# Kernel optimization log

Hardware: AMD Instinct MI355X
Metric: run time of the kernel (lower is better)

Reference implementation:

```python
import jax, jax.numpy as jnp
import numpy as np

K = 16          # knn neighbors (init kwarg k)
GROUPS = 4      # GroupNorm groups
EPS = 1e-5
SLOPE = 0.2     # LeakyReLU negative slope


def fps(xyz, n):
    """Farthest point sampling. xyz: (B,N,3) -> idx (B,n). First index is 0 (pointnet2 convention)."""
    B, N, _ = xyz.shape

    def step(carry, _):
        dist, last = carry
        p = jnp.take_along_axis(xyz, last[:, None, None], axis=1)  # (B,1,3)
        d = jnp.sum((xyz - p) ** 2, axis=-1)                       # (B,N)
        dist = jnp.minimum(dist, d)
        nxt = jnp.argmax(dist, axis=-1).astype(jnp.int32)
        return (dist, nxt), nxt

    init = (jnp.full((B, N), jnp.inf, xyz.dtype), jnp.zeros((B,), jnp.int32))
    _, idxs = jax.lax.scan(step, init, None, length=n - 1)  # (n-1, B)
    return jnp.concatenate([jnp.zeros((B, 1), jnp.int32), idxs.T], axis=1)


def graph_feature(cq, fq, ck, fk):
    """DGCNN edge features. cq:(B,Q,3) fq:(B,Q,C) ck:(B,N,3) fk:(B,N,C) -> (B,Q,K,2C)."""
    d2 = (jnp.sum(cq * cq, -1)[:, :, None]
          - 2.0 * jnp.einsum('bqc,bnc->bqn', cq, ck)
          + jnp.sum(ck * ck, -1)[:, None, :])        # (B,Q,N)
    _, idx = jax.lax.top_k(-d2, K)                    # (B,Q,K) nearest first
    nb = jax.vmap(lambda f_, i_: f_[i_])(fk, idx)     # (B,Q,K,C)
    ctr = jnp.broadcast_to(fq[:, :, None, :], nb.shape)
    return jnp.concatenate([nb - ctr, ctr], axis=-1)


def conv_gn_lrelu(y, W, gw, gb):
    """1x1 Conv2d (no bias) + GroupNorm(4) + LeakyReLU(0.2). y: (B,Q,K,Cin), W: (Cout,Cin)."""
    y = jnp.einsum('bqkc,oc->bqko', y, W)
    B, Q, Kk, C = y.shape
    yg = y.reshape(B, Q * Kk, GROUPS, C // GROUPS)
    m = yg.mean(axis=(1, 3), keepdims=True)
    v = yg.var(axis=(1, 3), keepdims=True)
    y = ((yg - m) * jax.lax.rsqrt(v + EPS)).reshape(B, Q, Kk, C) * gw + gb
    return jnp.where(y > 0, y, SLOPE * y)


def setup_inputs() -> dict:
    key = jax.random.key(0)
    ks = jax.random.split(key, 16)
    B, N = 8, 4096
    s = lambda k_, shape, scale=0.1: (jax.random.normal(k_, shape, jnp.float32) * scale)
    return {
        'x': jax.random.normal(ks[0], (B, N, 7), jnp.float32),
        'W_in': s(ks[1], (8, 3), 0.5), 'b_in': s(ks[2], (8,), 0.02),
        'W1': s(ks[3], (32, 16), 0.2), 'g1w': jnp.ones((32,), jnp.float32), 'g1b': jnp.zeros((32,), jnp.float32),
        'W2': s(ks[4], (64, 64), 0.1), 'g2w': jnp.ones((64,), jnp.float32), 'g2b': jnp.zeros((64,), jnp.float32),
        'W3': s(ks[5], (64, 128), 0.1), 'g3w': jnp.ones((64,), jnp.float32), 'g3b': jnp.zeros((64,), jnp.float32),
        'W4': s(ks[6], (128, 128), 0.1), 'g4w': jnp.ones((128,), jnp.float32), 'g4b': jnp.zeros((128,), jnp.float32),
        'num0': 1024,
    }


def reference(x, W_in, b_in, W1, g1w, g1b, W2, g2w, g2b, W3, g3w, g3b, W4, g4w, g4b, num0):
    coor, normal, plane = x[..., :3], x[..., 3:6], x[..., 6:7]   # (B,N,3),(B,N,3),(B,N,1)

    # input_trans: Conv1d(3,8,1)
    f = jnp.einsum('bnc,oc->bno', coor, W_in) + b_in             # (B,N,8)

    g = graph_feature(coor, f, coor, f)                          # (B,N,K,16)
    f = conv_gn_lrelu(g, W1, g1w, g1b).max(axis=2)               # (B,N,32)

    idx = fps(coor, num0)
    gather = lambda a: jnp.take_along_axis(a, idx[:, :, None], axis=1)
    coor_q, normal_q, plane_q, f_q = gather(coor), gather(normal), gather(plane), gather(f)

    g = graph_feature(coor_q, f_q, coor, f)                      # (B,num0,K,64)
    f = conv_gn_lrelu(g, W2, g2w, g2b).max(axis=2)               # (B,num0,64)
    coor, normal, plane = coor_q, normal_q, plane_q

    g = graph_feature(coor, f, coor, f)                          # (B,num0,K,128)
    f = conv_gn_lrelu(g, W3, g3w, g3b).max(axis=2)               # (B,num0,64)

    idx = fps(coor, num0)  # source uses num[0] again
    gather = lambda a: jnp.take_along_axis(a, idx[:, :, None], axis=1)
    coor_q, normal_q, plane_q, f_q = gather(coor), gather(normal), gather(plane), gather(f)

    g = graph_feature(coor_q, f_q, coor, f)                      # (B,num0,K,128)
    f = conv_gn_lrelu(g, W4, g4w, g4b).max(axis=2)               # (B,num0,128)

    return coor_q, f, normal_q, plane_q
```

## Files before the change

### kernel.cpp

```cpp
#include <hip/hip_runtime.h>
#include <cstdint>

static constexpr int B   = 8;
static constexpr int N0  = 4096;
static constexpr int NQ  = 1024;
static constexpr int KNB = 16;

__device__ __forceinline__ unsigned long long wave_max_u64_l63(unsigned long long k) {
#define STEPU_(ctrl)                                                                    \
  {                                                                                     \
    unsigned lo_ = (unsigned)k, hi_ = (unsigned)(k >> 32);                              \
    unsigned plo_ = (unsigned)__builtin_amdgcn_update_dpp((int)lo_, (int)lo_, ctrl,     \
                                                          0xf, 0xf, false);             \
    unsigned phi_ = (unsigned)__builtin_amdgcn_update_dpp((int)hi_, (int)hi_, ctrl,     \
                                                          0xf, 0xf, false);             \
    unsigned long long pk_ = ((unsigned long long)phi_ << 32) | plo_;                   \
    if (pk_ > k) k = pk_;                                                               \
  }
  STEPU_(0x111) STEPU_(0x112) STEPU_(0x114) STEPU_(0x118) STEPU_(0x142) STEPU_(0x143)
#undef STEPU_
  return k;
}

__global__ void prep_kernel(const float* __restrict__ x,
                            const float* __restrict__ W_in,
                            const float* __restrict__ b_in,
                            float4* __restrict__ c4, float* __restrict__ nrm,
                            float* __restrict__ pl, float* __restrict__ f0) {
  int i = blockIdx.x * 256 + threadIdx.x;
  if (i >= B * N0) return;
  const float* xp = x + (size_t)i * 7;
  float cx = xp[0], cy = xp[1], cz = xp[2];
  float kk = __fadd_rn(__fadd_rn(__fmul_rn(cx, cx), __fmul_rn(cy, cy)), __fmul_rn(cz, cz));
  c4[i] = make_float4(cx, cy, cz, kk);
  nrm[i * 3 + 0] = xp[3]; nrm[i * 3 + 1] = xp[4]; nrm[i * 3 + 2] = xp[5];
  pl[i] = xp[6];
#pragma unroll
  for (int o = 0; o < 8; o++) {
    f0[(size_t)i * 8 + o] = cx * W_in[o * 3 + 0] + cy * W_in[o * 3 + 1] + cz * W_in[o * 3 + 2] + b_in[o];
  }
}

template <int NC>
__device__ __forceinline__ void knn_body(int bq, int lane,
                                         const float4* __restrict__ q4,
                                         const float4* __restrict__ k4,
                                         int Q, int Nk, int* __restrict__ out) {
  int b = bq / Q;
  float4 q = q4[bq];
  const float4* kb = k4 + (size_t)b * Nk + lane;
  const float INF    = __int_as_float(0x7f800000);
  const float NEGINF = __int_as_float(0xff800000);
  float myd = INF;
  int   myi = 0;
  float kth = INF;
  const bool isl0 = (lane & 15) == 0;
  constexpr int G = (NC >= 8) ? 8 : NC;
  for (int c0 = 0; c0 < NC; c0 += G) {
    float dg[G];
#pragma unroll
    for (int u = 0; u < G; u++) {
      float4 kp = kb[(c0 + u) * 64];
      float dot = __fadd_rn(__fadd_rn(__fmul_rn(q.x, kp.x), __fmul_rn(q.y, kp.y)),
                            __fmul_rn(q.z, kp.z));
      dg[u] = __fadd_rn(__fsub_rn(q.w, __fmul_rn(2.0f, dot)), kp.w);
    }
#pragma unroll
    for (int u = 0; u < G; u++) {
      float d = dg[u];
      unsigned long long m = __ballot(d < kth);
      while (m) {
        int j = __builtin_ctzll(m);
        float dv = __int_as_float(__builtin_amdgcn_readlane(__float_as_int(d), j));
        int   iv = (c0 + u) * 64 + j;
        bool gt = (myd > dv);
        float pd = __int_as_float(__builtin_amdgcn_update_dpp(
            0, __float_as_int(myd), 0x111, 0xf, 0xf, true));
        int   pi = __builtin_amdgcn_update_dpp(0, myi, 0x111, 0xf, 0xf, true);
        pd = isl0 ? NEGINF : pd;
        bool tp = (pd > dv);
        float nd = tp ? pd : dv;
        int   ni = tp ? pi : iv;
        myd = gt ? nd : myd;
        myi = gt ? ni : myi;
        kth = __int_as_float(__builtin_amdgcn_readlane(__float_as_int(myd), 15));
        m = __ballot(d < kth);
        m = (j < 63) ? (m & (~0ull << (j + 1))) : 0ull;
      }
    }
  }
  if (lane < KNB) out[(size_t)bq * KNB + lane] = myi;
}

template <int CF, int CO>
__device__ __forceinline__ void ctry_body(int i, int total, const float* __restrict__ fq,
                                          const float* __restrict__ W,
                                          float* __restrict__ ctrY,
                                          const int* __restrict__ ridx, int Q, int Nsrc) {
  if (i >= total) return;
  int o = i % CO, bq = i / CO;
  const float* fp;
  if (ridx) {
    int b = bq / Q;
    fp = fq + ((size_t)b * Nsrc + ridx[bq]) * CF;
  } else {
    fp = fq + (size_t)bq * CF;
  }
  const float* wp = W + (size_t)o * (2 * CF) + CF;
  float acc = 0.f;
#pragma unroll
  for (int c = 0; c < CF; c++) acc = fmaf(fp[c], wp[c], acc);
  ctrY[i] = acc;
}

template <int NPTS>
__device__ __forceinline__ void fps_body(const float4* __restrict__ cb, int (&w)[4]) {
  constexpr int M = NPTS / 256;
  __shared__ __align__(16) float2 sxy[NPTS];
  __shared__ float szz[NPTS];
  __shared__ __align__(16) unsigned long long skey[2][4];
  const int tid = threadIdx.x;
  const int wid = tid >> 6, lane = tid & 63;
  float cx[M], cy[M], cz[M], dist[M];
#pragma unroll
  for (int i = 0; i < M; i++) {
    float4 p = cb[tid * M + i];
    cx[i] = p.x; cy[i] = p.y; cz[i] = p.z;
    dist[i] = 3.4e38f;
    sxy[tid * M + i] = make_float2(p.x, p.y);
    szz[tid * M + i] = p.z;
  }
  if (tid < 8) skey[tid >> 2][tid & 3] = 0ull;
  w[0] = w[1] = w[2] = w[3] = 0;
  float4 p0 = cb[0];
  float px = p0.x, py = p0.y, pz = p0.z;
  __syncthreads();
  for (int t = 1; t < NQ; t++) {
    float bv = -1.f; int bi = 0;
#pragma unroll
    for (int i = 0; i < M; i++) {
      float dx = __fsub_rn(cx[i], px), dy = __fsub_rn(cy[i], py), dz = __fsub_rn(cz[i], pz);
      float d = __fadd_rn(__fadd_rn(__fmul_rn(dx, dx), __fmul_rn(dy, dy)), __fmul_rn(dz, dz));
      float dd = dist[i]; dd = (d < dd) ? d : dd; dist[i] = dd;
      if (dd > bv) { bv = dd; bi = tid * M + i; }
    }
    unsigned long long k =
        ((unsigned long long)__float_as_uint(bv) << 12) | (unsigned)(4095 - bi);
    k = wave_max_u64_l63(k);
    const int par = t & 1;
    const unsigned long long tagbase = (unsigned long long)t << 44;
    if (lane == 63)
      __hip_atomic_store(&skey[par][wid], k | tagbase,
                         __ATOMIC_RELAXED, __HIP_MEMORY_SCOPE_WORKGROUP);
    unsigned long long k0, k1, k2, k3;
    do {
      k0 = __hip_atomic_load(&skey[par][0], __ATOMIC_RELAXED, __HIP_MEMORY_SCOPE_WORKGROUP);
      k1 = __hip_atomic_load(&skey[par][1], __ATOMIC_RELAXED, __HIP_MEMORY_SCOPE_WORKGROUP);
      k2 = __hip_atomic_load(&skey[par][2], __ATOMIC_RELAXED, __HIP_MEMORY_SCOPE_WORKGROUP);
      k3 = __hip_atomic_load(&skey[par][3], __ATOMIC_RELAXED, __HIP_MEMORY_SCOPE_WORKGROUP);
    } while (k0 < tagbase || k1 < tagbase || k2 < tagbase || k3 < tagbase);
    unsigned long long m0 = (k1 > k0) ? k1 : k0;
    unsigned long long m1 = (k3 > k2) ? k3 : k2;
    unsigned long long mk = (m1 > m0) ? m1 : m0;
    int win = 4095 - (int)(mk & 0xFFFull);
    float2 pxy = sxy[win];
    px = pxy.x; py = pxy.y; pz = szz[win];
    if (t == tid) w[0] = win;
    if (t == tid + 256) w[1] = win;
    if (t == tid + 512) w[2] = win;
    if (t == tid + 768) w[3] = win;
  }
}

template <int CF, int CO, int NT>
__device__ __forceinline__ void edgeconv_body(
    int blkid, const float* __restrict__ fq, const float* __restrict__ fk,
    const int* __restrict__ knn, const float* __restrict__ Wfull,
    const float* __restrict__ ctrY, const int* __restrict__ ridx,
    float* __restrict__ ymin, float* __restrict__ ymax,
    float* __restrict__ gstats, int Q, int Nk) {
  constexpr int J = CO / 4;
  constexpr int SEC = J * CF + 8;
  constexpr int NWARP = NT / 64;
  __shared__ float Wl[4 * SEC];
  __shared__ float sstat[8];
  for (int t = threadIdx.x; t < CO * CF; t += NT) {
    int o = t / CF, c = t % CF;
    Wl[(o / J) * SEC + (o % J) * CF + c] = Wfull[(size_t)o * (2 * CF) + c];
  }
  if (threadIdx.x < 8) sstat[threadIdx.x] = 0.0f;
  __syncthreads();
  const int wid = threadIdx.x >> 6, lane = threadIdx.x & 63;
  const int bq = blkid * NWARP + wid;
  const int b = bq / Q;
  const int g = lane >> 4, k = lane & 15;
  const int ni = knn[(size_t)bq * KNB + k];
  const float* nbp = fk + (size_t)(b * Nk + ni) * CF;
  const float* cp = ridx ? fq + ((size_t)b * Nk + ridx[bq]) * CF
                         : fq + (size_t)bq * CF;
  float acc[J];
#pragma unroll
  for (int j = 0; j < J; j++) acc[j] = 0.0f;
  const float* wg = &Wl[g * SEC];
#pragma unroll
  for (int c = 0; c < CF; c += 4) {
    float4 nb4 = *(const float4*)(nbp + c);
    float4 c4  = *(const float4*)(cp + c);
    float e0 = nb4.x - c4.x, e1 = nb4.y - c4.y, e2 = nb4.z - c4.z, e3 = nb4.w - c4.w;
#pragma unroll
    for (int j = 0; j < J; j++) {
      float4 w4 = *(const float4*)(wg + j * CF + c);
      acc[j] = fmaf(e0, w4.x, acc[j]);
      acc[j] = fmaf(e1, w4.y, acc[j]);
      acc[j] = fmaf(e2, w4.z, acc[j]);
      acc[j] = fmaf(e3, w4.w, acc[j]);
    }
  }
  float s = 0.f, s2 = 0.f;
  const float* cyp = ctrY + (size_t)bq * CO + g * J;
#pragma unroll
  for (int j = 0; j < J; j++) {
    float y = acc[j] + cyp[j];
    acc[j] = y;
    s += y; s2 = fmaf(y, y, s2);
  }
  float mn[J];
#pragma unroll
  for (int j = 0; j < J; j++) mn[j] = acc[j];
#pragma unroll
  for (int m = 1; m < 16; m <<= 1) {
#pragma unroll
    for (int j = 0; j < J; j++) {
      float a = __shfl_xor(acc[j], m); if (a > acc[j]) acc[j] = a;
      float c2 = __shfl_xor(mn[j], m); if (c2 < mn[j]) mn[j] = c2;
    }
    s  += __shfl_xor(s, m);
    s2 += __shfl_xor(s2, m);
  }
  if (k == 0) {
    float* mnp = ymin + (size_t)bq * CO + g * J;
    float* mxp = ymax + (size_t)bq * CO + g * J;
#pragma unroll
    for (int j = 0; j < J; j++) { mnp[j] = mn[j]; mxp[j] = acc[j]; }
    atomicAdd(&sstat[g], s);
    atomicAdd(&sstat[4 + g], s2);
  }
  __syncthreads();
  if (threadIdx.x < 8) atomicAdd(&gstats[b * 8 + threadIdx.x], sstat[threadIdx.x]);
}

__global__ __launch_bounds__(256, 2) void mega1_kernel(
    const float4* __restrict__ c40, const float* __restrict__ nrm,
    const float* __restrict__ pl, const float* __restrict__ f0,
    const float* __restrict__ W1, int* __restrict__ idx1,
    float4* __restrict__ c4q1, float* __restrict__ nq1, float* __restrict__ pq1,
    int* __restrict__ knn1, float* __restrict__ ctrY1) {
  int blk = blockIdx.x;
  if (blk < 8) {
    const int b = blk, tid = threadIdx.x;
    const float4* cb = c40 + (size_t)b * N0;
    int w[4];
    fps_body<N0>(cb, w);
    int* idxb = idx1 + (size_t)b * NQ;
#pragma unroll
    for (int u = 0; u < 4; u++) {
      int r = tid + u * 256;
      int s = (u == 0 && tid == 0) ? 0 : w[u];
      idxb[r] = s;
      c4q1[(size_t)b * NQ + r] = cb[s];
      const float* np = nrm + ((size_t)b * N0 + s) * 3;
      float* ndp = nq1 + ((size_t)b * NQ + r) * 3;
      ndp[0] = np[0]; ndp[1] = np[1]; ndp[2] = np[2];
      pq1[(size_t)b * NQ + r] = pl[(size_t)b * N0 + s];
    }
  } else if (blk < 8 + 8192) {
    int bq = (blk - 8) * 4 + (threadIdx.x >> 6);
    knn_body<64>(bq, threadIdx.x & 63, c40, c40, N0, N0, knn1);
  } else {
    int i = (blk - (8 + 8192)) * 256 + threadIdx.x;
    ctry_body<8, 32>(i, B * N0 * 32, f0, W1, ctrY1, nullptr, 0, 0);
  }
}

__global__ __launch_bounds__(256, 2) void ec1f_kernel(
    const float4* __restrict__ c4q1, const float* __restrict__ nq1,
    const float* __restrict__ pq1, const float* __restrict__ f0,
    const int* __restrict__ knn1, const float* __restrict__ W1,
    const float* __restrict__ ctrY1, float* __restrict__ ymin,
    float* __restrict__ ymax, float* __restrict__ gst1,
    int* __restrict__ idx2, float4* __restrict__ c4q2,
    float* __restrict__ cq2out, float* __restrict__ nq2out,
    float* __restrict__ pq2out) {
  int blk = blockIdx.x;
  if (blk < 8) {
    const int b = blk, tid = threadIdx.x;
    const float4* cqb = c4q1 + (size_t)b * NQ;
    int w[4];
    fps_body<NQ>(cqb, w);
    int* idxb = idx2 + (size_t)b * NQ;
#pragma unroll
    for (int u = 0; u < 4; u++) {
      int r = tid + u * 256;
      int s = (u == 0 && tid == 0) ? 0 : w[u];
      idxb[r] = s;
      float4 c = cqb[s];
      c4q2[(size_t)b * NQ + r] = c;
      float* cd = cq2out + ((size_t)b * NQ + r) * 3;
      cd[0] = c.x; cd[1] = c.y; cd[2] = c.z;
      const float* np = nq1 + ((size_t)b * NQ + s) * 3;
      float* ndp = nq2out + ((size_t)b * NQ + r) * 3;
      ndp[0] = np[0]; ndp[1] = np[1]; ndp[2] = np[2];
      pq2out[(size_t)b * NQ + r] = pq1[(size_t)b * NQ + s];
    }
  } else {
    edgeconv_body<8, 32, 256>(blk - 8, f0, f0, knn1, W1, ctrY1, nullptr,
                              ymin, ymax, gst1, N0, N0);
  }
}

__global__ __launch_bounds__(256, 2) void mega2_kernel(
    const float4* __restrict__ c40, const float4* __restrict__ c4q1,
    const float* __restrict__ f1, const int* __restrict__ idx1,
    const float* __restrict__ W2,
    int* __restrict__ knn2, int* __restrict__ knn3, float* __restrict__ ctrY2) {
  int blk = blockIdx.x;
  if (blk < 2048) {
    int bq = blk * 4 + (threadIdx.x >> 6);
    knn_body<64>(bq, threadIdx.x & 63, c4q1, c40, NQ, N0, knn2);
  } else if (blk < 4096) {
    int bq = (blk - 2048) * 4 + (threadIdx.x >> 6);
    knn_body<16>(bq, threadIdx.x & 63, c4q1, c4q1, NQ, NQ, knn3);
  } else {
    int i = (blk - 4096) * 256 + threadIdx.x;
    ctry_body<32, 64>(i, B * NQ * 64, f1, W2, ctrY2, idx1, NQ, N0);
  }
}

__global__ __launch_bounds__(256, 4) void mega3_kernel(
    const float4* __restrict__ c4q1, const float4* __restrict__ c4q2,
    const float* __restrict__ f3, const int* __restrict__ idx2,
    const float* __restrict__ W4, int* __restrict__ knn4, float* __restrict__ ctrY4) {
  int blk = blockIdx.x;
  if (blk < 2048) {
    int bq = blk * 4 + (threadIdx.x >> 6);
    knn_body<16>(bq, threadIdx.x & 63, c4q2, c4q1, NQ, NQ, knn4);
  } else {
    int i = (blk - 2048) * 256 + threadIdx.x;
    ctry_body<64, 128>(i, B * NQ * 128, f3, W4, ctrY4, idx2, NQ, NQ);
  }
}

template <int CF, int CO>
__global__ void ctry_kernel(const float* __restrict__ fq, const float* __restrict__ W,
                            float* __restrict__ ctrY, int total) {
  int i = blockIdx.x * 256 + threadIdx.x;
  ctry_body<CF, CO>(i, total, fq, W, ctrY, nullptr, 0, 0);
}

template <int CF, int CO>
__global__ __launch_bounds__(256) void edgeconv_kernel(
    const float* __restrict__ fq, const float* __restrict__ fk,
    const int* __restrict__ knn, const float* __restrict__ Wfull,
    const float* __restrict__ ctrY, const int* __restrict__ ridx,
    float* __restrict__ ymin, float* __restrict__ ymax,
    float* __restrict__ gstats, int Q, int Nk) {
  edgeconv_body<CF, CO, 256>(blockIdx.x, fq, fk, knn, Wfull, ctrY, ridx,
                             ymin, ymax, gstats, Q, Nk);
}

template <int CO>
__global__ void gn_out_kernel(const float* __restrict__ ymin, const float* __restrict__ ymax,
                              const float* __restrict__ gstats, const float* __restrict__ gw,
                              const float* __restrict__ gb, float* __restrict__ fout,
                              int total, int Q, float inv_cnt) {
  int i = blockIdx.x * 256 + threadIdx.x;
  if (i >= total) return;
  constexpr int J = CO / 4;
  int o = i % CO; int bq = i / CO; int b = bq / Q;
  int g = o / J;
  float m  = gstats[b * 8 + g] * inv_cnt;
  float s2 = gstats[b * 8 + 4 + g] * inv_cnt;
  float rs = rsqrtf(s2 - m * m + 1e-5f);
  float sc = gw[o] * rs;
  float sel = (sc >= 0.f) ? ymax[i] : ymin[i];
  float v = (sel - m) * sc + gb[o];
  fout[i] = (v > 0.f) ? v : 0.2f * v;
}

extern "C" void kernel_launch(void* const* d_in, const int* in_sizes, int n_in,
                              void* d_out, int out_size, void* d_ws, size_t ws_size,
                              hipStream_t stream) {
  (void)in_sizes; (void)n_in; (void)out_size; (void)ws_size;
  const float* x    = (const float*)d_in[0];
  const float* W_in = (const float*)d_in[1];
  const float* b_in = (const float*)d_in[2];
  const float* W1   = (const float*)d_in[3];
  const float* g1w  = (const float*)d_in[4];
  const float* g1b  = (const float*)d_in[5];
  const float* W2   = (const float*)d_in[6];
  const float* g2w  = (const float*)d_in[7];
  const float* g2b  = (const float*)d_in[8];
  const float* W3   = (const float*)d_in[9];
  const float* g3w  = (const float*)d_in[10];
  const float* g3b  = (const float*)d_in[11];
  const float* W4   = (const float*)d_in[12];
  const float* g4w  = (const float*)d_in[13];
  const float* g4b  = (const float*)d_in[14];

  float* ws = (float*)d_ws;
  size_t o_c40  = 0;
  size_t o_nrm  = o_c40  + (size_t)B * N0 * 4;
  size_t o_pl   = o_nrm  + (size_t)B * N0 * 3;
  size_t o_f0   = o_pl   + (size_t)B * N0;
  size_t o_f1   = o_f0   + (size_t)B * N0 * 8;
  size_t o_ctrY = o_f1   + (size_t)B * N0 * 32;
  size_t o_ymin = o_ctrY + (size_t)B * N0 * 32;
  size_t o_ymax = o_ymin + (size_t)B * N0 * 32;
  size_t o_knnA = o_ymax + (size_t)B * N0 * 32;
  size_t o_knnB = o_knnA + (size_t)B * N0 * KNB;
  size_t o_gst  = o_knnB + (size_t)B * NQ * KNB;
  size_t o_idx1 = o_gst  + 4 * B * 8;
  size_t o_idx2 = o_idx1 + (size_t)B * NQ;
  size_t o_c4q1 = o_idx2 + (size_t)B * NQ;
  size_t o_c4q2 = o_c4q1 + (size_t)B * NQ * 4;
  size_t o_nq1  = o_c4q2 + (size_t)B * NQ * 4;
  size_t o_pq1  = o_nq1  + (size_t)B * NQ * 3;
  size_t o_f2   = o_pq1  + (size_t)B * NQ;
  size_t o_f3   = o_f2   + (size_t)B * NQ * 64;

  float4* c40  = (float4*)(ws + o_c40);
  float*  nrm  = ws + o_nrm;   float* pl   = ws + o_pl;
  float*  f0   = ws + o_f0;    float* f1   = ws + o_f1;
  float*  ctrY = ws + o_ctrY;  float* ymin = ws + o_ymin;  float* ymax = ws + o_ymax;
  int*    knnA = (int*)(ws + o_knnA);
  int*    knnB = (int*)(ws + o_knnB);
  float*  gst  = ws + o_gst;
  int*    idx1 = (int*)(ws + o_idx1);
  int*    idx2 = (int*)(ws + o_idx2);
  float4* c4q1 = (float4*)(ws + o_c4q1);
  float4* c4q2 = (float4*)(ws + o_c4q2);
  float*  nq1  = ws + o_nq1;   float* pq1  = ws + o_pq1;
  float*  f2   = ws + o_f2;    float* f3   = ws + o_f3;

  float* out  = (float*)d_out;
  float* cq2  = out;
  float* fout = out + (size_t)B * NQ * 3;
  float* nq2  = fout + (size_t)B * NQ * 128;
  float* pq2  = nq2 + (size_t)B * NQ * 3;

  hipMemsetAsync(gst, 0, 4 * B * 8 * sizeof(float), stream);

  prep_kernel<<<(B * N0 + 255) / 256, 256, 0, stream>>>(x, W_in, b_in, c40, nrm, pl, f0);

  mega1_kernel<<<8 + 8192 + 4096, 256, 0, stream>>>(c40, nrm, pl, f0, W1,
                                                    idx1, c4q1, nq1, pq1, knnA, ctrY);
  ec1f_kernel<<<8 + 8192, 256, 0, stream>>>(c4q1, nq1, pq1, f0, knnA, W1, ctrY,
                                            ymin, ymax, gst + 0,
                                            idx2, c4q2, cq2, nq2, pq2);
  gn_out_kernel<32><<<(B * N0 * 32 + 255) / 256, 256, 0, stream>>>(
      ymin, ymax, gst + 0, g1w, g1b, f1, B * N0 * 32, N0, 1.0f / (4096.0f * 16.0f * 8.0f));

  mega2_kernel<<<2048 + 2048 + 2048, 256, 0, stream>>>(
      c40, c4q1, f1, idx1, W2, knnA, knnB, ctrY);
  edgeconv_kernel<32, 64><<<B * NQ / 4, 256, 0, stream>>>(f1, f1, knnA, W2, ctrY, idx1,
                                                          ymin, ymax, gst + B * 8, NQ, N0);
  gn_out_kernel<64><<<(B * NQ * 64 + 255) / 256, 256, 0, stream>>>(
      ymin, ymax, gst + B * 8, g2w, g2b, f2, B * NQ * 64, NQ, 1.0f / (1024.0f * 16.0f * 16.0f));

  ctry_kernel<64, 64><<<(B * NQ * 64 + 255) / 256, 256, 0, stream>>>(f2, W3, ctrY, B * NQ * 64);
  edgeconv_kernel<64, 64><<<B * NQ / 4, 256, 0, stream>>>(f2, f2, knnB, W3, ctrY, nullptr,
                                                          ymin, ymax, gst + 2 * B * 8, NQ, NQ);
  gn_out_kernel<64><<<(B * NQ * 64 + 255) / 256, 256, 0, stream>>>(
      ymin, ymax, gst + 2 * B * 8, g3w, g3b, f3, B * NQ * 64, NQ, 1.0f / (1024.0f * 16.0f * 16.0f));

  mega3_kernel<<<2048 + 4096, 256, 0, stream>>>(c4q1, c4q2, f3, idx2, W4, knnB, ctrY);
  edgeconv_kernel<64, 128><<<B * NQ / 4, 256, 0, stream>>>(f3, f3, knnB, W4, ctrY, idx2,
                                                           ymin, ymax, gst + 3 * B * 8, NQ, NQ);
  gn_out_kernel<128><<<(B * NQ * 128 + 255) / 256, 256, 0, stream>>>(
      ymin, ymax, gst + 3 * B * 8, g4w, g4b, fout, B * NQ * 128, NQ, 1.0f / (1024.0f * 16.0f * 32.0f));
}
```

Before: 1.694 ms.

## Run second FPS on a single wavefront and use barrier-based reduction in the first

The second farthest-point-sampling stage (1024 points) now runs on one 64-lane wavefront with 16 points per lane. Each iteration's argmax comes from a DPP wave reduction plus readlane, so no cross-wave communication is needed. Winners are stored in shared memory and gathered afterwards. The generic 256-thread FPS also replaces its spin-wait atomic handshake with a __syncthreads-based reduction. This trades per-iteration inter-wave synchronization for more serial work per lane, and leaves the other three waves of those blocks idle.

```diff
diff --git a/kernel.cpp b/kernel.cpp
--- a/kernel.cpp
+++ b/kernel.cpp
@@ -114,11 +114,13 @@
 }
 
 template <int NPTS>
-__device__ __forceinline__ void fps_body(const float4* __restrict__ cb, int (&w)[4]) {
-  constexpr int M = NPTS / 256;
+__device__ __forceinline__ void fps_body(const float4* __restrict__ cb, int* w) {
+  constexpr int BLK = 256;
+  constexpr int M = NPTS / BLK;
+  constexpr int NW = BLK / 64;
   __shared__ __align__(16) float2 sxy[NPTS];
   __shared__ float szz[NPTS];
-  __shared__ __align__(16) unsigned long long skey[2][4];
+  __shared__ __align__(16) unsigned long long skey[2][NW];
   const int tid = threadIdx.x;
   const int wid = tid >> 6, lane = tid & 63;
   float cx[M], cy[M], cz[M], dist[M];
@@ -130,7 +132,6 @@
     sxy[tid * M + i] = make_float2(p.x, p.y);
     szz[tid * M + i] = p.z;
   }
-  if (tid < 8) skey[tid >> 2][tid & 3] = 0ull;
   w[0] = w[1] = w[2] = w[3] = 0;
   float4 p0 = cb[0];
   float px = p0.x, py = p0.y, pz = p0.z;
@@ -147,21 +148,14 @@
     unsigned long long k =
         ((unsigned long long)__float_as_uint(bv) << 12) | (unsigned)(4095 - bi);
     k = wave_max_u64_l63(k);
-    const int par = t & 1;
-    const unsigned long long tagbase = (unsigned long long)t << 44;
-    if (lane == 63)
-      __hip_atomic_store(&skey[par][wid], k | tagbase,
-                         __ATOMIC_RELAXED, __HIP_MEMORY_SCOPE_WORKGROUP);
-    unsigned long long k0, k1, k2, k3;
-    do {
-      k0 = __hip_atomic_load(&skey[par][0], __ATOMIC_RELAXED, __HIP_MEMORY_SCOPE_WORKGROUP);
-      k1 = __hip_atomic_load(&skey[par][1], __ATOMIC_RELAXED, __HIP_MEMORY_SCOPE_WORKGROUP);
-      k2 = __hip_atomic_load(&skey[par][2], __ATOMIC_RELAXED, __HIP_MEMORY_SCOPE_WORKGROUP);
-      k3 = __hip_atomic_load(&skey[par][3], __ATOMIC_RELAXED, __HIP_MEMORY_SCOPE_WORKGROUP);
-    } while (k0 < tagbase || k1 < tagbase || k2 < tagbase || k3 < tagbase);
-    unsigned long long m0 = (k1 > k0) ? k1 : k0;
-    unsigned long long m1 = (k3 > k2) ? k3 : k2;
-    unsigned long long mk = (m1 > m0) ? m1 : m0;
+    int p = t & 1;
+    if (lane == 63) skey[p][wid] = k;
+    __syncthreads();
+    ulonglong2 ab = *(const ulonglong2*)&skey[p][0];
+    ulonglong2 cd = *(const ulonglong2*)&skey[p][2];
+    unsigned long long m0 = (ab.x > ab.y) ? ab.x : ab.y;
+    unsigned long long m1 = (cd.x > cd.y) ? cd.x : cd.y;
+    unsigned long long mk = (m0 > m1) ? m0 : m1;
     int win = 4095 - (int)(mk & 0xFFFull);
     float2 pxy = sxy[win];
     px = pxy.x; py = pxy.y; pz = szz[win];
@@ -169,6 +163,44 @@
     if (t == tid + 256) w[1] = win;
     if (t == tid + 512) w[2] = win;
     if (t == tid + 768) w[3] = win;
+  }
+}
+
+template <int NPTS>
+__device__ __forceinline__ void fps1w_body(const float4* __restrict__ cb,
+                                           float2* __restrict__ sxy,
+                                           float* __restrict__ szz,
+                                           int* __restrict__ swin) {
+  constexpr int M = NPTS / 64;
+  const int lane = threadIdx.x;
+  float cx[M], cy[M], cz[M], dist[M];
+#pragma unroll
+  for (int i = 0; i < M; i++) {
+    float4 p = cb[lane * M + i];
+    cx[i] = p.x; cy[i] = p.y; cz[i] = p.z;
+    dist[i] = 3.4e38f;
+    sxy[lane * M + i] = make_float2(p.x, p.y);
+    szz[lane * M + i] = p.z;
+  }
+  float4 p0 = cb[0];
+  float px = p0.x, py = p0.y, pz = p0.z;
+  for (int t = 1; t < NQ; t++) {
+    float bv = -1.f; int bi = 0;
+#pragma unroll
+    for (int i = 0; i < M; i++) {
+      float dx = __fsub_rn(cx[i], px), dy = __fsub_rn(cy[i], py), dz = __fsub_rn(cz[i], pz);
+      float d = __fadd_rn(__fadd_rn(__fmul_rn(dx, dx), __fmul_rn(dy, dy)), __fmul_rn(dz, dz));
+      float dd = dist[i]; dd = (d < dd) ? d : dd; dist[i] = dd;
+      if (dd > bv) { bv = dd; bi = lane * M + i; }
+    }
+    unsigned long long k =
+        ((unsigned long long)__float_as_uint(bv) << 12) | (unsigned)(4095 - bi);
+    k = wave_max_u64_l63(k);
+    unsigned klo = (unsigned)__builtin_amdgcn_readlane((int)(unsigned)k, 63);
+    int win = 4095 - (int)(klo & 0xFFFu);
+    if (lane == 0) swin[t] = win;
+    float2 pxy = sxy[win];
+    px = pxy.x; py = pxy.y; pz = szz[win];
   }
 }
 
@@ -293,24 +325,28 @@
     float* __restrict__ pq2out) {
   int blk = blockIdx.x;
   if (blk < 8) {
-    const int b = blk, tid = threadIdx.x;
-    const float4* cqb = c4q1 + (size_t)b * NQ;
-    int w[4];
-    fps_body<NQ>(cqb, w);
-    int* idxb = idx2 + (size_t)b * NQ;
-#pragma unroll
-    for (int u = 0; u < 4; u++) {
-      int r = tid + u * 256;
-      int s = (u == 0 && tid == 0) ? 0 : w[u];
-      idxb[r] = s;
-      float4 c = cqb[s];
-      c4q2[(size_t)b * NQ + r] = c;
-      float* cd = cq2out + ((size_t)b * NQ + r) * 3;
-      cd[0] = c.x; cd[1] = c.y; cd[2] = c.z;
-      const float* np = nq1 + ((size_t)b * NQ + s) * 3;
-      float* ndp = nq2out + ((size_t)b * NQ + r) * 3;
-      ndp[0] = np[0]; ndp[1] = np[1]; ndp[2] = np[2];
-      pq2out[(size_t)b * NQ + r] = pq1[(size_t)b * NQ + s];
+    if (threadIdx.x < 64) {
+      __shared__ __align__(16) float2 sxy2[NQ];
+      __shared__ float szz2[NQ];
+      __shared__ int swin2[NQ];
+      const int b = blk, lane = threadIdx.x;
+      const float4* cqb = c4q1 + (size_t)b * NQ;
+      fps1w_body<NQ>(cqb, sxy2, szz2, swin2);
+      int* idxb = idx2 + (size_t)b * NQ;
+#pragma unroll
+      for (int u = 0; u < NQ / 64; u++) {
+        int r = lane + u * 64;
+        int s = (r == 0) ? 0 : swin2[r];
+        idxb[r] = s;
+        float4 c = cqb[s];
+        c4q2[(size_t)b * NQ + r] = c;
+        float* cd = cq2out + ((size_t)b * NQ + r) * 3;
+        cd[0] = c.x; cd[1] = c.y; cd[2] = c.z;
+        const float* np = nq1 + ((size_t)b * NQ + s) * 3;
+        float* ndp = nq2out + ((size_t)b * NQ + r) * 3;
+        ndp[0] = np[0]; ndp[1] = np[1]; ndp[2] = np[2];
+        pq2out[(size_t)b * NQ + r] = pq1[(size_t)b * NQ + s];
+      }
     }
   } else {
     edgeconv_body<8, 32, 256>(blk - 8, f0, f0, knn1, W1, ctrY1, nullptr,
```

Result: faster. 1.617 ms (-4.6%).
